# Optimization experiments

Measured on AMD Instinct MI355X. Metric: run time of the kernel, lower is better.

## Reference

```python
import jax, jax.numpy as jnp
import numpy as np

B, S, D = 4, 4096, 64

def setup_inputs() -> dict:
    key = jax.random.key(0)
    kq, kk, kv = jax.random.split(key, 3)
    return {
        "q": jax.random.normal(kq, (B, S, D), dtype=jnp.float32),
        "k": jax.random.normal(kk, (B, S, D), dtype=jnp.float32),
        "v": jax.random.normal(kv, (B, S, D), dtype=jnp.float32),
    }

def reference(q, k, v):
    # scores: [B, Sq, Sk]; NOTE: scale is k.shape[-1] (not sqrt), per the source.
    scores = jnp.einsum("bqd,bkd->bqk", q, k) / k.shape[-1]
    # softmax over dim=1 == the QUERY axis (non-standard), then matmul V.
    probs = jax.nn.softmax(scores, axis=1)            # [B, Sq, Sk]
    attn = jnp.einsum("bqk,bkd->bqd", probs, v)       # [B, Sq, D]
    attn_w = jax.nn.softmax(attn, axis=1)             # softmax over Sq again
    return (attn, attn_w)
```

## Files before the change

kernel.cpp:

```cpp
#include <hip/hip_runtime.h>
#include <hip/hip_bf16.h>
#include <math.h>

#define BB 4
#define SS 4096
#define DD 64
#define KSPLIT 4
#define QSPLIT 16

typedef __attribute__((ext_vector_type(8))) short short8;
typedef __attribute__((ext_vector_type(4))) float f32x4;
typedef __attribute__((ext_vector_type(2))) unsigned int u32x2;
typedef unsigned int u32;
typedef unsigned short ushort_t;

#define MFMA32(a,b,c) __builtin_amdgcn_mfma_f32_16x16x32_bf16((a),(b),(c),0,0,0)
#define C2SC 0.022542110700140054f

#define BAR() do { asm volatile("" ::: "memory"); \
                   __builtin_amdgcn_s_barrier();  \
                   asm volatile("" ::: "memory"); } while (0)
#define WAIT_VM(N)  asm volatile("s_waitcnt vmcnt(" #N ")" ::: "memory")
#define DS_FENCE() do { asm volatile("s_waitcnt lgkmcnt(0)" ::: "memory"); \
                        __builtin_amdgcn_sched_barrier(0); } while (0)

union Pk8 { short8 s8; u32 u[4]; u32x2 h[2]; };

static __device__ __forceinline__ unsigned short f2bf(float f) {
  union { float f; u32 u; } x; x.f = f;
  u32 r = (x.u + 0x7FFFu + ((x.u >> 16) & 1u)) >> 16;
  return (unsigned short)r;
}

static __device__ __forceinline__ u32 pk2(float a, float b) {
  __hip_bfloat16 lo = __float2bfloat16(a);
  __hip_bfloat16 hi = __float2bfloat16(b);
  unsigned short ls, hs;
  __builtin_memcpy(&ls, &lo, 2); __builtin_memcpy(&hs, &hi, 2);
  return (u32)ls | ((u32)hs << 16);
}

static __device__ __forceinline__ void gload16(const void* g, void* l) {
  __builtin_amdgcn_global_load_lds((const __attribute__((address_space(1))) u32*)g,
                                   (__attribute__((address_space(3))) u32*)l, 16, 0, 0);
}

__global__ __launch_bounds__(256) void p0_convert(
    const float* __restrict__ q, const float* __restrict__ k,
    ushort_t* __restrict__ QB, ushort_t* __restrict__ KB,
    float* __restrict__ out0, float* __restrict__ z2)
{
  const size_t i = (size_t)blockIdx.x * 256 + threadIdx.x;
  float4 a = ((const float4*)q)[i];
  float4 c = ((const float4*)k)[i];
  ((ushort4*)QB)[i] = make_ushort4(f2bf(a.x*C2SC), f2bf(a.y*C2SC), f2bf(a.z*C2SC), f2bf(a.w*C2SC));
  ((ushort4*)KB)[i] = make_ushort4(f2bf(c.x), f2bf(c.y), f2bf(c.z), f2bf(c.w));
  ((float4*)out0)[i] = make_float4(0.f, 0.f, 0.f, 0.f);
  if (blockIdx.x == 0) z2[threadIdx.x] = 0.f;
}

__global__ __launch_bounds__(256) void pa_colsum(
    const ushort_t* __restrict__ QB, const ushort_t* __restrict__ KB,
    float* __restrict__ Zp)
{
  const int kb0 = blockIdx.x * 128;
  const int qch = blockIdx.y;
  const int b   = blockIdx.z;
  const int t = threadIdx.x, w = t >> 6, lane = t & 63;
  const int g = lane >> 4, r15 = lane & 15;
  const int QCH = SS / QSPLIT;
  const int NT = QCH / 64;

  __shared__ alignas(16) char qbuf[2][64*128];

  short8 ak[2][2];
#pragma unroll
  for (int s = 0; s < 2; ++s)
#pragma unroll
    for (int dh = 0; dh < 2; ++dh)
      ak[s][dh] = *(const short8*)(KB + ((size_t)b*SS + kb0 + 32*w + 16*s + r15)*DD + 32*dh + 8*g);

  const int q0g = qch * QCH;
#define PA_STAGE(tt, buf) do {                                              \
    _Pragma("unroll")                                                       \
    for (int j = 0; j < 2; ++j) {                                           \
      const int row = 16*w + 8*j + (lane >> 3);                             \
      const char* gsrc = (const char*)(QB + ((size_t)b*SS + q0g + (tt)*64 + row)*DD) \
                         + 16*((lane & 7) ^ (row & 7));                     \
      gload16(gsrc, qbuf[buf] + (16*w + 8*j)*128);                          \
    }                                                                       \
  } while (0)

  PA_STAGE(0, 0);

  float z[8];
#pragma unroll
  for (int i = 0; i < 8; ++i) z[i] = 0.f;

#pragma unroll 1
  for (int tt = 0; tt < NT; ++tt) {
    if (tt < NT-1) {
      PA_STAGE(tt+1, (tt+1)&1);
      WAIT_VM(2);
    } else {
      WAIT_VM(0);
    }
    BAR();
    const char* qb = qbuf[tt & 1];
#pragma unroll
    for (int qt = 0; qt < 4; ++qt) {
      const int qrow = 16*qt + r15;
      const char* base = qb + qrow*128;
      short8 bq0 = *(const short8*)(base + 16*((g    ) ^ (qrow & 7)));
      short8 bq1 = *(const short8*)(base + 16*((4 + g) ^ (qrow & 7)));
#pragma unroll
      for (int s = 0; s < 2; ++s) {
        f32x4 a = {0.f,0.f,0.f,0.f};
        a = MFMA32(ak[s][0], bq0, a);
        a = MFMA32(ak[s][1], bq1, a);
        z[4*s+0] += exp2f(a[0]); z[4*s+1] += exp2f(a[1]);
        z[4*s+2] += exp2f(a[2]); z[4*s+3] += exp2f(a[3]);
      }
    }
    DS_FENCE();
    BAR();
  }
#undef PA_STAGE

#pragma unroll
  for (int m = 1; m < 16; m <<= 1)
#pragma unroll
    for (int i = 0; i < 8; ++i) z[i] += __shfl_xor(z[i], m);
  if (r15 == 0) {
#pragma unroll
    for (int s = 0; s < 2; ++s)
#pragma unroll
      for (int r = 0; r < 4; ++r)
        Zp[((size_t)qch*BB + b)*SS + kb0 + 32*w + 16*s + 4*g + r] = z[4*s+r];
  }
}

__global__ __launch_bounds__(256) void p2_vt(
    const float* __restrict__ v, const float* __restrict__ Zp,
    ushort_t* __restrict__ VT)
{
  const int k0 = blockIdx.x * 64;
  const int b  = blockIdx.y;
  const int t = threadIdx.x;
  __shared__ float vs[64][65];
  __shared__ float izs[64];
  {
    const int row = t >> 2, cq = (t & 3) * 16;
    const float* src = v + ((size_t)b*SS + k0 + row)*DD + cq;
#pragma unroll
    for (int i = 0; i < 4; ++i) {
      float4 x = ((const float4*)src)[i];
      vs[row][cq + 4*i + 0] = x.x; vs[row][cq + 4*i + 1] = x.y;
      vs[row][cq + 4*i + 2] = x.z; vs[row][cq + 4*i + 3] = x.w;
    }
  }
  if (t < 64) {
    float z = 0.f;
#pragma unroll
    for (int c = 0; c < QSPLIT; ++c)
      z += Zp[((size_t)c*BB + b)*SS + k0 + t];
    izs[t] = 1.0f / z;
  }
  __syncthreads();
  const int d = t >> 2, ks = (t & 3) * 16;
  u32* dst = (u32*)VT + (((size_t)b*DD + d)*SS + k0 + ks)/2;
#pragma unroll
  for (int i = 0; i < 8; ++i) {
    float a0 = vs[ks + 2*i    ][d] * izs[ks + 2*i    ];
    float a1 = vs[ks + 2*i + 1][d] * izs[ks + 2*i + 1];
    dst[i] = (u32)f2bf(a0) | ((u32)f2bf(a1) << 16);
  }
}

template<int MODE>
__global__ __launch_bounds__(256) void pb_attn(
    const ushort_t* __restrict__ QB, const ushort_t* __restrict__ KB,
    const ushort_t* __restrict__ VT, float* __restrict__ outp)
{
  const int qbase = blockIdx.x * 32;
  const int ky = blockIdx.y;
  const int kbase = ky * (SS / KSPLIT);
  const int b  = blockIdx.z;
  const int t = threadIdx.x, w = t >> 6, lane = t & 63;
  const int g = lane >> 4, r15 = lane & 15;
  const int wk = w >> 1, qs = w & 1;
  const int NT = SS / KSPLIT / 64;

  __shared__ alignas(16) char smem[32768];

  short8 aq[2];
#pragma unroll
  for (int dh = 0; dh < 2; ++dh)
    aq[dh] = *(const short8*)(QB + ((size_t)b*SS + qbase + 16*qs + r15)*DD + 32*dh + 8*g);

  f32x4 acc[4];
#pragma unroll
  for (int dt = 0; dt < 4; ++dt) acc[dt] = (f32x4){0.f,0.f,0.f,0.f};

#define PB_STAGE(kt, buf) do {                                               \
    const int kc = kbase + (kt)*64;                                          \
    _Pragma("unroll")                                                        \
    for (int j = 0; j < 2; ++j) {                                            \
      const int row = 16*w + 8*j + (lane >> 3);                              \
      const char* gk = (const char*)(KB + ((size_t)b*SS + kc + row)*DD)      \
                       + 16*((lane & 7) ^ (row & 7));                        \
      gload16(gk, smem + (buf)*16384 + (16*w + 8*j)*128);                    \
    }                                                                        \
    _Pragma("unroll")                                                        \
    for (int j = 0; j < 2; ++j) {                                            \
      const int row = 16*w + 8*j + (lane >> 3);                              \
      const char* gv = (const char*)(VT + ((size_t)b*DD + row)*SS + kc)      \
                       + 16*((lane & 7) ^ (row & 7));                        \
      gload16(gv, smem + (buf)*16384 + 8192 + (16*w + 8*j)*128);             \
    }                                                                        \
  } while (0)

  PB_STAGE(0, 0);

#pragma unroll 1
  for (int kt = 0; kt < NT; ++kt) {
    if (kt < NT-1) {
      PB_STAGE(kt+1, (kt+1)&1);
      WAIT_VM(4);
    } else {
      WAIT_VM(0);
    }
    BAR();
    const char* kb = smem + (kt&1)*16384;
    const char* vb = kb + 8192;

    u32 pku[2][2];
#pragma unroll
    for (int s = 0; s < 2; ++s) {
      const int rowA = 32*wk + 16*s + r15;
      const char* base = kb + rowA*128;
      short8 ka0 = *(const short8*)(base + 16*((g    ) ^ (r15 & 7)));
      short8 ka1 = *(const short8*)(base + 16*((4 + g) ^ (r15 & 7)));
      f32x4 a = {0.f,0.f,0.f,0.f};
      a = MFMA32(ka0, aq[0], a);
      a = MFMA32(ka1, aq[1], a);
      pku[s][0] = pk2(exp2f(a[0]), exp2f(a[1]));
      pku[s][1] = pk2(exp2f(a[2]), exp2f(a[3]));
    }
    Pk8 ap;
    ap.u[0] = pku[0][0]; ap.u[1] = pku[0][1];
    ap.u[2] = pku[1][0]; ap.u[3] = pku[1][1];

    short8 bv[4];
#pragma unroll
    for (int dt = 0; dt < 4; ++dt) {
      const int vrow = 16*dt + r15;
      Pk8 u;
      u.h[0] = *(const u32x2*)(vb + vrow*128 + 16*((4*wk     + (g>>1)) ^ (r15 & 7)) + 8*(g&1));
      u.h[1] = *(const u32x2*)(vb + vrow*128 + 16*((4*wk + 2 + (g>>1)) ^ (r15 & 7)) + 8*(g&1));
      bv[dt] = u.s8;
    }
#pragma unroll
    for (int dt = 0; dt < 4; ++dt)
      acc[dt] = MFMA32(ap.s8, bv[dt], acc[dt]);
    DS_FENCE();
    BAR();
  }
#undef PB_STAGE

  f32x4* red = (f32x4*)smem;
  if (wk == 1) {
#pragma unroll
    for (int dt = 0; dt < 4; ++dt) red[(qs*4 + dt)*64 + lane] = acc[dt];
  }
  __syncthreads();
  if (wk == 0) {
    float* dst = (MODE == 0) ? outp : outp + (size_t)ky * BB * SS * DD;
#pragma unroll
    for (int dt = 0; dt < 4; ++dt) {
      f32x4 s = acc[dt] + red[(qs*4 + dt)*64 + lane];
#pragma unroll
      for (int rr = 0; rr < 4; ++rr) {
        const size_t idx = ((size_t)b*SS + qbase + 16*qs + 4*g + rr)*DD + 16*dt + r15;
        if (MODE == 0) atomicAdd(&outp[idx], s[rr]);
        else           dst[idx] = s[rr];
      }
    }
  }
}

__global__ __launch_bounds__(256) void k4f(
    const float* __restrict__ attn, float* __restrict__ z2)
{
  const int b = blockIdx.x;
  const int q0 = blockIdx.y * 32;
  const int t = threadIdx.x;
  const int d = t & 63, rg = t >> 6;
  float ze = 0.f;
#pragma unroll
  for (int i = 0; i < 8; ++i) {
    float a = attn[((size_t)b*SS + q0 + 4*i + rg)*DD + d];
    ze += __expf(a);
  }
  __shared__ float red[4][64];
  red[rg][d] = ze;
  __syncthreads();
  if (t < 64)
    atomicAdd(&z2[b*DD + t], red[0][t] + red[1][t] + red[2][t] + red[3][t]);
}

__global__ __launch_bounds__(256) void k5_comb(
    const float* __restrict__ parts, float* __restrict__ out0, float* __restrict__ z2)
{
  const int b = blockIdx.x;
  const int q0 = blockIdx.y * 32;
  const int t = threadIdx.x;
  const int d = t & 63, rg = t >> 6;
  const size_t N = (size_t)BB * SS * DD;
  float ze = 0.f;
#pragma unroll
  for (int i = 0; i < 8; ++i) {
    const size_t idx = ((size_t)b*SS + q0 + 4*i + rg)*DD + d;
    float a = parts[idx] + parts[N + idx] + parts[2*N + idx] + parts[3*N + idx];
    out0[idx] = a;
    ze += __expf(a);
  }
  __shared__ float red[4][64];
  red[rg][d] = ze;
  __syncthreads();
  if (t < 64)
    atomicAdd(&z2[b*DD + t], red[0][t] + red[1][t] + red[2][t] + red[3][t]);
}

__global__ __launch_bounds__(256) void k6w(
    const float* __restrict__ attn, const float* __restrict__ z2,
    float* __restrict__ out1)
{
  const size_t i = (size_t)blockIdx.x * 256 + threadIdx.x;
  const int b = (int)(i >> 18);
  const int d = (int)(i & 63);
  out1[i] = __expf(attn[i]) / z2[b*DD + d];
}

extern "C" void kernel_launch(void* const* d_in, const int* in_sizes, int n_in,
                              void* d_out, int out_size, void* d_ws, size_t ws_size,
                              hipStream_t stream) {
  const float* q = (const float*)d_in[0];
  const float* k = (const float*)d_in[1];
  const float* v = (const float*)d_in[2];
  float* out0 = (float*)d_out;
  float* out1 = out0 + (size_t)BB * SS * DD;

  ushort_t* QB = (ushort_t*)out1;
  ushort_t* KB = QB + (size_t)BB * SS * DD;

  char* ws = (char*)d_ws;
  ushort_t* VT = (ushort_t*)ws;
  float* Zp = (float*)(ws + (size_t)BB*DD*SS*2);
  float* z2 = Zp + (size_t)QSPLIT * BB * SS;
  float* parts = z2 + 256;

  const size_t need = (size_t)BB*DD*SS*2 + (size_t)QSPLIT*BB*SS*4 + 1024
                    + (size_t)KSPLIT*BB*SS*DD*4;
  const bool use_parts = (ws_size >= need);

  hipLaunchKernelGGL(p0_convert, dim3(BB*SS*DD/4/256), dim3(256), 0, stream, q, k, QB, KB, out0, z2);
  hipLaunchKernelGGL(pa_colsum, dim3(SS/128, QSPLIT, BB), dim3(256), 0, stream, QB, KB, Zp);
  hipLaunchKernelGGL(p2_vt, dim3(SS/64, BB), dim3(256), 0, stream, v, Zp, VT);
  if (use_parts) {
    pb_attn<1><<<dim3(SS/32, KSPLIT, BB), dim3(256), 0, stream>>>(QB, KB, VT, parts);
    hipLaunchKernelGGL(k5_comb, dim3(BB, SS/32), dim3(256), 0, stream, parts, out0, z2);
  } else {
    pb_attn<0><<<dim3(SS/32, KSPLIT, BB), dim3(256), 0, stream>>>(QB, KB, VT, out0);
    hipLaunchKernelGGL(k4f, dim3(BB, SS/32), dim3(256), 0, stream, out0, z2);
  }
  hipLaunchKernelGGL(k6w, dim3(BB*SS*DD/256), dim3(256), 0, stream, out0, z2, out1);
}
```

Measured before the change: 87.94 us.

## Widen attention block to 128 queries to reuse staged K/V tiles

```diff
diff --git a/kernel.cpp b/kernel.cpp
--- a/kernel.cpp
+++ b/kernel.cpp
@@ -6,7 +6,7 @@
 #define SS 4096
 #define DD 64
 #define KSPLIT 4
-#define QSPLIT 16
+#define QSPLIT 4
 
 typedef __attribute__((ext_vector_type(8))) short short8;
 typedef __attribute__((ext_vector_type(4))) float f32x4;
@@ -36,7 +36,8 @@
   __hip_bfloat16 lo = __float2bfloat16(a);
   __hip_bfloat16 hi = __float2bfloat16(b);
   unsigned short ls, hs;
-  __builtin_memcpy(&ls, &lo, 2); __builtin_memcpy(&hs, &hi, 2);
+  __builtin_memcpy(&ls, &lo, 2); __builtin_memcpy(&hs, &hs, 0);
+  __builtin_memcpy(&hs, &hi, 2);
   return (u32)ls | ((u32)hs << 16);
 }
 
@@ -182,7 +183,7 @@
     const ushort_t* __restrict__ QB, const ushort_t* __restrict__ KB,
     const ushort_t* __restrict__ VT, float* __restrict__ outp)
 {
-  const int qbase = blockIdx.x * 32;
+  const int qbase = blockIdx.x * 128;
   const int ky = blockIdx.y;
   const int kbase = ky * (SS / KSPLIT);
   const int b  = blockIdx.z;
@@ -193,14 +194,18 @@
 
   __shared__ alignas(16) char smem[32768];
 
-  short8 aq[2];
-#pragma unroll
-  for (int dh = 0; dh < 2; ++dh)
-    aq[dh] = *(const short8*)(QB + ((size_t)b*SS + qbase + 16*qs + r15)*DD + 32*dh + 8*g);
-
-  f32x4 acc[4];
-#pragma unroll
-  for (int dt = 0; dt < 4; ++dt) acc[dt] = (f32x4){0.f,0.f,0.f,0.f};
+  short8 aq[4][2];
+#pragma unroll
+  for (int qt = 0; qt < 4; ++qt)
+#pragma unroll
+    for (int dh = 0; dh < 2; ++dh)
+      aq[qt][dh] = *(const short8*)(QB + ((size_t)b*SS + qbase + 64*qs + 16*qt + r15)*DD + 32*dh + 8*g);
+
+  f32x4 acc[4][4];
+#pragma unroll
+  for (int qt = 0; qt < 4; ++qt)
+#pragma unroll
+    for (int dt = 0; dt < 4; ++dt) acc[qt][dt] = (f32x4){0.f,0.f,0.f,0.f};
 
 #define PB_STAGE(kt, buf) do {                                               \
     const int kc = kbase + (kt)*64;                                          \
@@ -234,23 +239,22 @@
     const char* kb = smem + (kt&1)*16384;
     const char* vb = kb + 8192;
 
-    u32 pku[2][2];
+    u32 pku[2][4][2];
 #pragma unroll
     for (int s = 0; s < 2; ++s) {
       const int rowA = 32*wk + 16*s + r15;
       const char* base = kb + rowA*128;
       short8 ka0 = *(const short8*)(base + 16*((g    ) ^ (r15 & 7)));
       short8 ka1 = *(const short8*)(base + 16*((4 + g) ^ (r15 & 7)));
-      f32x4 a = {0.f,0.f,0.f,0.f};
-      a = MFMA32(ka0, aq[0], a);
-      a = MFMA32(ka1, aq[1], a);
-      pku[s][0] = pk2(exp2f(a[0]), exp2f(a[1]));
-      pku[s][1] = pk2(exp2f(a[2]), exp2f(a[3]));
-    }
-    Pk8 ap;
-    ap.u[0] = pku[0][0]; ap.u[1] = pku[0][1];
-    ap.u[2] = pku[1][0]; ap.u[3] = pku[1][1];
-
+#pragma unroll
+      for (int qt = 0; qt < 4; ++qt) {
+        f32x4 a = {0.f,0.f,0.f,0.f};
+        a = MFMA32(ka0, aq[qt][0], a);
+        a = MFMA32(ka1, aq[qt][1], a);
+        pku[s][qt][0] = pk2(exp2f(a[0]), exp2f(a[1]));
+        pku[s][qt][1] = pk2(exp2f(a[2]), exp2f(a[3]));
+      }
+    }
     short8 bv[4];
 #pragma unroll
     for (int dt = 0; dt < 4; ++dt) {
@@ -261,8 +265,14 @@
       bv[dt] = u.s8;
     }
 #pragma unroll
-    for (int dt = 0; dt < 4; ++dt)
-      acc[dt] = MFMA32(ap.s8, bv[dt], acc[dt]);
+    for (int qt = 0; qt < 4; ++qt) {
+      Pk8 ap;
+      ap.u[0] = pku[0][qt][0]; ap.u[1] = pku[0][qt][1];
+      ap.u[2] = pku[1][qt][0]; ap.u[3] = pku[1][qt][1];
+#pragma unroll
+      for (int dt = 0; dt < 4; ++dt)
+        acc[qt][dt] = MFMA32(ap.s8, bv[dt], acc[qt][dt]);
+    }
     DS_FENCE();
     BAR();
   }
@@ -271,21 +281,25 @@
   f32x4* red = (f32x4*)smem;
   if (wk == 1) {
 #pragma unroll
-    for (int dt = 0; dt < 4; ++dt) red[(qs*4 + dt)*64 + lane] = acc[dt];
+    for (int qt = 0; qt < 4; ++qt)
+#pragma unroll
+      for (int dt = 0; dt < 4; ++dt) red[(qs*16 + qt*4 + dt)*64 + lane] = acc[qt][dt];
   }
   __syncthreads();
   if (wk == 0) {
     float* dst = (MODE == 0) ? outp : outp + (size_t)ky * BB * SS * DD;
 #pragma unroll
-    for (int dt = 0; dt < 4; ++dt) {
-      f32x4 s = acc[dt] + red[(qs*4 + dt)*64 + lane];
-#pragma unroll
-      for (int rr = 0; rr < 4; ++rr) {
-        const size_t idx = ((size_t)b*SS + qbase + 16*qs + 4*g + rr)*DD + 16*dt + r15;
-        if (MODE == 0) atomicAdd(&outp[idx], s[rr]);
-        else           dst[idx] = s[rr];
+    for (int qt = 0; qt < 4; ++qt)
+#pragma unroll
+      for (int dt = 0; dt < 4; ++dt) {
+        f32x4 s = acc[qt][dt] + red[(qs*16 + qt*4 + dt)*64 + lane];
+#pragma unroll
+        for (int rr = 0; rr < 4; ++rr) {
+          const size_t idx = ((size_t)b*SS + qbase + 64*qs + 16*qt + 4*g + rr)*DD + 16*dt + r15;
+          if (MODE == 0) atomicAdd(&outp[idx], s[rr]);
+          else           dst[idx] = s[rr];
+        }
       }
-    }
   }
 }
 
@@ -368,10 +382,10 @@
   hipLaunchKernelGGL(pa_colsum, dim3(SS/128, QSPLIT, BB), dim3(256), 0, stream, QB, KB, Zp);
   hipLaunchKernelGGL(p2_vt, dim3(SS/64, BB), dim3(256), 0, stream, v, Zp, VT);
   if (use_parts) {
-    pb_attn<1><<<dim3(SS/32, KSPLIT, BB), dim3(256), 0, stream>>>(QB, KB, VT, parts);
+    pb_attn<1><<<dim3(SS/128, KSPLIT, BB), dim3(256), 0, stream>>>(QB, KB, VT, parts);
     hipLaunchKernelGGL(k5_comb, dim3(BB, SS/32), dim3(256), 0, stream, parts, out0, z2);
   } else {
-    pb_attn<0><<<dim3(SS/32, KSPLIT, BB), dim3(256), 0, stream>>>(QB, KB, VT, out0);
+    pb_attn<0><<<dim3(SS/128, KSPLIT, BB), dim3(256), 0, stream>>>(QB, KB, VT, out0);
     hipLaunchKernelGGL(k4f, dim3(BB, SS/32), dim3(256), 0, stream, out0, z2);
   }
   hipLaunchKernelGGL(k6w, dim3(BB*SS*DD/256), dim3(256), 0, stream, out0, z2, out1);
```

Result: faster. 85.35 us (-2.9%).
